# Optimization experiments

Hardware: AMD Instinct MI355X
Metric: run time of the kernel (lower is better)

The kernel has to match this reference:

```python
import jax, jax.numpy as jnp
import numpy as np


def setup_inputs() -> dict:
    key = jax.random.key(0)
    k1, k2, k3, k4 = jax.random.split(key, 4)
    tokens, d_in, d_out = 8192, 4096, 4096
    x = jax.random.normal(k1, (tokens, d_in), dtype=jnp.float32)
    # int8-valued weights stored as int32 for portability; values in [-128, 127]
    quantized_weights = jax.random.randint(k2, (d_out, d_in), -128, 128, dtype=jnp.int32)
    scales = jax.random.uniform(k3, (d_out,), dtype=jnp.float32) * 0.02 + 1e-4
    bias = jax.random.normal(k4, (d_out,), dtype=jnp.float32)
    return {"x": x, "quantized_weights": quantized_weights, "scales": scales, "bias": bias}


def reference(x, quantized_weights, scales, bias):
    # dequantize-on-the-fly linear: (x @ W_q^T) * scales + bias
    w = quantized_weights.astype(x.dtype)                # [out, in]
    out = jnp.einsum('ti,oi->to', x, w)                  # [tokens, out]
    out = out * scales[None, :].astype(x.dtype)
    out = out + bias.astype(x.dtype)
    return out
```

## Files before the change

### kernel.cpp

```cpp
#include <hip/hip_runtime.h>
#include <stdint.h>

#define M_TOK 8192
#define N_OUT 4096
#define K_IN  4096

#define BM 256
#define BN 256
#define BK 128
#define NT (K_IN / BK)
#define SEC 16384
#define BUF 65536

typedef int intx4 __attribute__((ext_vector_type(4)));

#define MFMAI8 __builtin_amdgcn_mfma_i32_16x16x64_i8


__device__ __forceinline__ void async_copy16(const void* g, void* l) {
    __builtin_amdgcn_global_load_lds(
        (__attribute__((address_space(1))) void*)(g),
        (__attribute__((address_space(3))) void*)(l),
        16, 0, 0);
}


#define NWB 4096

__global__ void prep_kernel(const float* __restrict__ x,
                            const int* __restrict__ wq,
                            int8_t* __restrict__ xq,
                            float* __restrict__ sx,
                            int8_t* __restrict__ wb) {
    const int tid = threadIdx.x;

    if (blockIdx.x < M_TOK) {
        const int row = blockIdx.x;
        const float4* p = (const float4*)(x + (size_t)row * K_IN + tid * 16);
        float4 v0 = p[0], v1 = p[1], v2 = p[2], v3 = p[3];

        float m = fabsf(v0.x);
        m = fmaxf(m, fabsf(v0.y)); m = fmaxf(m, fabsf(v0.z)); m = fmaxf(m, fabsf(v0.w));
        m = fmaxf(m, fabsf(v1.x)); m = fmaxf(m, fabsf(v1.y));
        m = fmaxf(m, fabsf(v1.z)); m = fmaxf(m, fabsf(v1.w));
        m = fmaxf(m, fabsf(v2.x)); m = fmaxf(m, fabsf(v2.y));
        m = fmaxf(m, fabsf(v2.z)); m = fmaxf(m, fabsf(v2.w));
        m = fmaxf(m, fabsf(v3.x)); m = fmaxf(m, fabsf(v3.y));
        m = fmaxf(m, fabsf(v3.z)); m = fmaxf(m, fabsf(v3.w));

#pragma unroll
        for (int off = 32; off; off >>= 1) m = fmaxf(m, __shfl_xor(m, off));
        __shared__ float wmax[4];
        if ((tid & 63) == 0) wmax[tid >> 6] = m;
        __syncthreads();
        m = fmaxf(fmaxf(wmax[0], wmax[1]), fmaxf(wmax[2], wmax[3]));
        m = fmaxf(m, 1e-20f);

        const float rs = 127.0f / m;
        if (tid == 0) sx[row] = m * (1.0f / 127.0f);

        union { int4 v; int8_t c[16]; } u;
        u.c[0]  = (int8_t)__float2int_rn(v0.x * rs);
        u.c[1]  = (int8_t)__float2int_rn(v0.y * rs);
        u.c[2]  = (int8_t)__float2int_rn(v0.z * rs);
        u.c[3]  = (int8_t)__float2int_rn(v0.w * rs);
        u.c[4]  = (int8_t)__float2int_rn(v1.x * rs);
        u.c[5]  = (int8_t)__float2int_rn(v1.y * rs);
        u.c[6]  = (int8_t)__float2int_rn(v1.z * rs);
        u.c[7]  = (int8_t)__float2int_rn(v1.w * rs);
        u.c[8]  = (int8_t)__float2int_rn(v2.x * rs);
        u.c[9]  = (int8_t)__float2int_rn(v2.y * rs);
        u.c[10] = (int8_t)__float2int_rn(v2.z * rs);
        u.c[11] = (int8_t)__float2int_rn(v2.w * rs);
        u.c[12] = (int8_t)__float2int_rn(v3.x * rs);
        u.c[13] = (int8_t)__float2int_rn(v3.y * rs);
        u.c[14] = (int8_t)__float2int_rn(v3.z * rs);
        u.c[15] = (int8_t)__float2int_rn(v3.w * rs);
        ((int4*)(xq + (size_t)row * K_IN))[tid] = u.v;
    } else {
        const int i = (blockIdx.x - M_TOK) * 256 + tid;
        const int4* p = (const int4*)wq + (size_t)i * 4;
        int4 a = p[0], b = p[1], c = p[2], d = p[3];
        union { int4 v; int8_t q[16]; } u;
        u.q[0]  = (int8_t)a.x; u.q[1]  = (int8_t)a.y; u.q[2]  = (int8_t)a.z; u.q[3]  = (int8_t)a.w;
        u.q[4]  = (int8_t)b.x; u.q[5]  = (int8_t)b.y; u.q[6]  = (int8_t)b.z; u.q[7]  = (int8_t)b.w;
        u.q[8]  = (int8_t)c.x; u.q[9]  = (int8_t)c.y; u.q[10] = (int8_t)c.z; u.q[11] = (int8_t)c.w;
        u.q[12] = (int8_t)d.x; u.q[13] = (int8_t)d.y; u.q[14] = (int8_t)d.z; u.q[15] = (int8_t)d.w;
        ((int4*)wb)[i] = u.v;
    }
}


__global__ __launch_bounds__(512, 2)
void gemm_i8_kernel(const int8_t* __restrict__ A,
                    const int8_t* __restrict__ B,
                    const float* __restrict__ sx,
                    const float* __restrict__ scales,
                    const float* __restrict__ bias,
                    float* __restrict__ C) {
    __shared__ __align__(16) int8_t lds[2 * BUF];

    const int tid = threadIdx.x;

    const int nwg = (M_TOK / BM) * (N_OUT / BN);
    const int cpx = nwg / 8;
    const int wg  = (blockIdx.x % 8) * cpx + blockIdx.x / 8;
    const int bn  = wg & 15;
    const int bm  = wg >> 4;

    const int lane = tid & 63;
    const int wave = tid >> 6;
    const int wm   = wave >> 2;
    const int wn   = wave & 3;

    const int t8 = tid >> 3;
    const int cg = (tid & 7) ^ (t8 & 7);
    const int grow0 = 2 * t8 + (cg >> 2);
    const int gcol0 = (cg & 3) * 16;
    const int8_t* aP = A + (size_t)(bm * BM + grow0) * K_IN + gcol0;
    const int8_t* bP = B + (size_t)(bn * BN + grow0) * K_IN + gcol0;

    auto stA = [&](int tt, int s) {
        int8_t* d = &lds[(tt & 1) * BUF + s * SEC + tid * 16];
        const int8_t* g = aP + (size_t)tt * BK + s * 64;
        async_copy16(g, d);
        async_copy16(g + (size_t)128 * K_IN, d + 8192);
    };
    auto stB = [&](int tt, int s) {
        int8_t* d = &lds[(tt & 1) * BUF + 2 * SEC + s * SEC + tid * 16];
        const int8_t* g = bP + (size_t)tt * BK + s * 64;
        async_copy16(g, d);
        async_copy16(g + (size_t)128 * K_IN, d + 8192);
    };

    const int r16 = lane & 15;
    const int q   = lane >> 4;
    const int cr  = (((r16 & 1) << 2) + q) ^ ((r16 >> 1) & 7);
    const int aOff = (wm * 64 + (r16 >> 1)) * 128 + cr * 16;
    const int bOff = 2 * SEC + (wn * 32 + (r16 >> 1)) * 128 + cr * 16;

    intx4 acc[8][4] = {};
    intx4 afA[4], afB[4], bfA[4], bfB[4];

#define RD_A03(dst, base, s)                                                   \
    { _Pragma("unroll") for (int i = 0; i < 4; ++i)                            \
        dst[i] = *(const intx4*)((base) + (s) * SEC + aOff + i * 1024); }
#define RD_A47(dst, base, s)                                                   \
    { _Pragma("unroll") for (int i = 0; i < 4; ++i)                            \
        dst[i] = *(const intx4*)((base) + (s) * SEC + aOff + (4 + i) * 1024); }
#define RD_BF(dst, base, s)                                                    \
    { _Pragma("unroll") for (int j = 0; j < 4; ++j)                            \
        dst[j] = *(const intx4*)((base) + (s) * SEC + bOff + j * 1024); }
#define MM03(af, bf)                                                           \
    { __builtin_amdgcn_s_setprio(1);                                           \
      _Pragma("unroll") for (int i = 0; i < 4; ++i)                            \
          _Pragma("unroll") for (int j = 0; j < 4; ++j)                        \
              acc[i][j] = MFMAI8(af[i], bf[j], acc[i][j], 0, 0, 0);            \
      __builtin_amdgcn_s_setprio(0); }
#define MM47(af, bf)                                                           \
    { __builtin_amdgcn_s_setprio(1);                                           \
      _Pragma("unroll") for (int i = 0; i < 4; ++i)                            \
          _Pragma("unroll") for (int j = 0; j < 4; ++j)                        \
              acc[4 + i][j] = MFMAI8(af[i], bf[j], acc[4 + i][j], 0, 0, 0);    \
      __builtin_amdgcn_s_setprio(0); }
#define SBAR __builtin_amdgcn_sched_barrier(0)

    stA(0, 0); stB(0, 0); stA(0, 1); stB(0, 1);
    asm volatile("s_waitcnt vmcnt(0)" ::: "memory");
    __builtin_amdgcn_s_barrier();
    asm volatile("" ::: "memory");
    RD_A03(afA, lds, 0);
    RD_BF(bfA, lds, 0);

#pragma unroll 1
    for (int t = 0; t < NT; ++t) {
        const int8_t* Lb  = lds + (t & 1) * BUF;
        const int8_t* Lb2 = lds + ((t + 1) & 1) * BUF;
        const bool pf = (t + 1 < NT);

        if (pf) { stA(t + 1, 0); stA(t + 1, 1); }
        RD_A47(afB, Lb, 0);
        asm volatile("s_waitcnt lgkmcnt(4)" ::: "memory");
        SBAR;
        MM03(afA, bfA);

        if (pf) { stB(t + 1, 0); stB(t + 1, 1); }
        RD_A03(afA, Lb, 1);
        RD_BF(bfB, Lb, 1);
        asm volatile("s_waitcnt lgkmcnt(8)" ::: "memory");
        SBAR;
        MM47(afB, bfA);

        RD_A47(afB, Lb, 1);
        asm volatile("s_waitcnt lgkmcnt(4)" ::: "memory");
        SBAR;
        MM03(afA, bfB);

        asm volatile("s_waitcnt vmcnt(0) lgkmcnt(0)" ::: "memory");
        __builtin_amdgcn_s_barrier();
        asm volatile("" ::: "memory");
        if (pf) {
            RD_A03(afA, Lb2, 0);
            RD_BF(bfA, Lb2, 0);
        }
        SBAR;
        MM47(afB, bfB);
    }

    const int row0 = bm * BM + wm * 128 + q * 4;
    const int col0 = bn * BN + wn * 64 + r16;
    float sxv[8][4];
#pragma unroll
    for (int fr = 0; fr < 8; ++fr)
#pragma unroll
        for (int r = 0; r < 4; ++r)
            sxv[fr][r] = sx[row0 + fr * 16 + r];
#pragma unroll
    for (int fc = 0; fc < 4; ++fc) {
        const int n  = col0 + fc * 16;
        const float sc = scales[n];
        const float bi = bias[n];
#pragma unroll
        for (int fr = 0; fr < 8; ++fr) {
            const int m = row0 + fr * 16;
#pragma unroll
            for (int r = 0; r < 4; ++r)
                C[(size_t)(m + r) * N_OUT + n] =
                    (float)acc[fr][fc][r] * (sxv[fr][r] * sc) + bi;
        }
    }
}


extern "C" void kernel_launch(void* const* d_in, const int* in_sizes, int n_in,
                              void* d_out, int out_size, void* d_ws, size_t ws_size,
                              hipStream_t stream) {
    const float* x      = (const float*)d_in[0];
    const int*   wq     = (const int*)d_in[1];
    const float* scales = (const float*)d_in[2];
    const float* bias   = (const float*)d_in[3];
    float*       out    = (float*)d_out;

    int8_t* xq = (int8_t*)d_ws;
    int8_t* wb = xq + (size_t)M_TOK * K_IN;
    float*  sx = (float*)(wb + (size_t)N_OUT * K_IN);

    prep_kernel<<<M_TOK + NWB, 256, 0, stream>>>(x, wq, xq, sx, wb);

    const int grid = (M_TOK / BM) * (N_OUT / BN);
    gemm_i8_kernel<<<grid, 512, 0, stream>>>(xq, wb, sx, scales, bias, out);
}
```

Measured before the change: 188.6 us.

## Switch int8 GEMM to 32x32x32 MFMA with new LDS slice layout

Replaces the 16x16x64 int8 MFMA tiles with 32x32x32 int8 MFMA instructions, using 4x2 accumulators of 16 ints per wave in place of 8x4 of 4. The LDS staging is reorganised into four 32-byte K-slices per operand, with a new XOR swizzle and per-lane read offsets matched to the larger fragment shape. The epilogue now reads sx per element instead of preloading it. The intent is to cut instruction issue overhead and raise MFMA throughput per LDS read, at the risk of new bank conflicts and scattered epilogue loads.

New measurement: 224.8 us. 19.2% more time.

```diff
diff --git a/kernel.cpp b/kernel.cpp
--- a/kernel.cpp
+++ b/kernel.cpp
@@ -9,12 +9,14 @@
 #define BN 256
 #define BK 128
 #define NT (K_IN / BK)
-#define SEC 16384
-#define BUF 65536
-
-typedef int intx4 __attribute__((ext_vector_type(4)));
-
-#define MFMAI8 __builtin_amdgcn_mfma_i32_16x16x64_i8
+#define SLICE 8192
+#define BSEC  32768
+#define BUF   65536
+
+typedef int intx4  __attribute__((ext_vector_type(4)));
+typedef int intx16 __attribute__((ext_vector_type(16)));
+
+#define MFMA32 __builtin_amdgcn_mfma_i32_32x32x32_i8
 
 
 __device__ __forceinline__ void async_copy16(const void* g, void* l) {
@@ -113,64 +115,53 @@
     const int wm   = wave >> 2;
     const int wn   = wave & 3;
 
-    const int t8 = tid >> 3;
-    const int cg = (tid & 7) ^ (t8 & 7);
-    const int grow0 = 2 * t8 + (cg >> 2);
-    const int gcol0 = (cg & 3) * 16;
-    const int8_t* aP = A + (size_t)(bm * BM + grow0) * K_IN + gcol0;
-    const int8_t* bP = B + (size_t)(bn * BN + grow0) * K_IN + gcol0;
+    const int grow0 = ((tid >> 6) << 5) + ((tid >> 1) & 31);
+    const int gc0   = (((tid & 1) ^ ((tid >> 3) & 1)) << 4);
+    const int8_t* aP = A + (size_t)(bm * BM + grow0) * K_IN + gc0;
+    const int8_t* bP = B + (size_t)(bn * BN + grow0) * K_IN + gc0;
 
     auto stA = [&](int tt, int s) {
-        int8_t* d = &lds[(tt & 1) * BUF + s * SEC + tid * 16];
-        const int8_t* g = aP + (size_t)tt * BK + s * 64;
-        async_copy16(g, d);
-        async_copy16(g + (size_t)128 * K_IN, d + 8192);
+        async_copy16(aP + (size_t)tt * BK + s * 32,
+                     &lds[(tt & 1) * BUF + s * SLICE + tid * 16]);
     };
     auto stB = [&](int tt, int s) {
-        int8_t* d = &lds[(tt & 1) * BUF + 2 * SEC + s * SEC + tid * 16];
-        const int8_t* g = bP + (size_t)tt * BK + s * 64;
-        async_copy16(g, d);
-        async_copy16(g + (size_t)128 * K_IN, d + 8192);
+        async_copy16(bP + (size_t)tt * BK + s * 32,
+                     &lds[(tt & 1) * BUF + BSEC + s * SLICE + tid * 16]);
     };
 
-    const int r16 = lane & 15;
-    const int q   = lane >> 4;
-    const int cr  = (((r16 & 1) << 2) + q) ^ ((r16 >> 1) & 7);
-    const int aOff = (wm * 64 + (r16 >> 1)) * 128 + cr * 16;
-    const int bOff = 2 * SEC + (wn * 32 + (r16 >> 1)) * 128 + cr * 16;
-
-    intx4 acc[8][4] = {};
+    const int aRd = ((lane & 31) << 5) + ((((lane >> 5) ^ (lane >> 2)) & 1) << 4);
+    const int hi  = lane >> 5;
+
+    intx16 acc[4][2] = {};
     intx4 afA[4], afB[4], bfA[4], bfB[4];
 
-#define RD_A03(dst, base, s)                                                   \
-    { _Pragma("unroll") for (int i = 0; i < 4; ++i)                            \
-        dst[i] = *(const intx4*)((base) + (s) * SEC + aOff + i * 1024); }
-#define RD_A47(dst, base, s)                                                   \
-    { _Pragma("unroll") for (int i = 0; i < 4; ++i)                            \
-        dst[i] = *(const intx4*)((base) + (s) * SEC + aOff + (4 + i) * 1024); }
-#define RD_BF(dst, base, s)                                                    \
-    { _Pragma("unroll") for (int j = 0; j < 4; ++j)                            \
-        dst[j] = *(const intx4*)((base) + (s) * SEC + bOff + j * 1024); }
-#define MM03(af, bf)                                                           \
+#define RD_A(dst, base, sp, f0)                                                \
+    { _Pragma("unroll") for (int fr = 0; fr < 2; ++fr)                         \
+        _Pragma("unroll") for (int ss = 0; ss < 2; ++ss)                       \
+            dst[fr * 2 + ss] = *(const intx4*)((base) +                        \
+                ((sp) * 2 + ss) * SLICE + (wm * 4 + (f0) + fr) * 1024 + aRd); }
+#define RD_B(dst, base, sp)                                                    \
+    { _Pragma("unroll") for (int fc = 0; fc < 2; ++fc)                         \
+        _Pragma("unroll") for (int ss = 0; ss < 2; ++ss)                       \
+            dst[fc * 2 + ss] = *(const intx4*)((base) + BSEC +                 \
+                ((sp) * 2 + ss) * SLICE + (wn * 2 + fc) * 1024 + aRd); }
+#define MM(af, bf, a0)                                                         \
     { __builtin_amdgcn_s_setprio(1);                                           \
-      _Pragma("unroll") for (int i = 0; i < 4; ++i)                            \
-          _Pragma("unroll") for (int j = 0; j < 4; ++j)                        \
-              acc[i][j] = MFMAI8(af[i], bf[j], acc[i][j], 0, 0, 0);            \
-      __builtin_amdgcn_s_setprio(0); }
-#define MM47(af, bf)                                                           \
-    { __builtin_amdgcn_s_setprio(1);                                           \
-      _Pragma("unroll") for (int i = 0; i < 4; ++i)                            \
-          _Pragma("unroll") for (int j = 0; j < 4; ++j)                        \
-              acc[4 + i][j] = MFMAI8(af[i], bf[j], acc[4 + i][j], 0, 0, 0);    \
+      _Pragma("unroll") for (int fr = 0; fr < 2; ++fr)                         \
+          _Pragma("unroll") for (int fc = 0; fc < 2; ++fc)                     \
+              _Pragma("unroll") for (int ss = 0; ss < 2; ++ss)                 \
+                  acc[(a0) + fr][fc] = MFMA32(af[fr * 2 + ss],                 \
+                      bf[fc * 2 + ss], acc[(a0) + fr][fc], 0, 0, 0);           \
       __builtin_amdgcn_s_setprio(0); }
 #define SBAR __builtin_amdgcn_sched_barrier(0)
 
-    stA(0, 0); stB(0, 0); stA(0, 1); stB(0, 1);
+    stA(0, 0); stA(0, 1); stA(0, 2); stA(0, 3);
+    stB(0, 0); stB(0, 1); stB(0, 2); stB(0, 3);
     asm volatile("s_waitcnt vmcnt(0)" ::: "memory");
     __builtin_amdgcn_s_barrier();
     asm volatile("" ::: "memory");
-    RD_A03(afA, lds, 0);
-    RD_BF(bfA, lds, 0);
+    RD_A(afA, lds, 0, 0);
+    RD_B(bfA, lds, 0);
 
 #pragma unroll 1
     for (int t = 0; t < NT; ++t) {
@@ -178,55 +169,51 @@
         const int8_t* Lb2 = lds + ((t + 1) & 1) * BUF;
         const bool pf = (t + 1 < NT);
 
-        if (pf) { stA(t + 1, 0); stA(t + 1, 1); }
-        RD_A47(afB, Lb, 0);
+        if (pf) { stA(t + 1, 0); stA(t + 1, 1); stA(t + 1, 2); stA(t + 1, 3); }
+        RD_A(afB, Lb, 0, 2);
         asm volatile("s_waitcnt lgkmcnt(4)" ::: "memory");
         SBAR;
-        MM03(afA, bfA);
-
-        if (pf) { stB(t + 1, 0); stB(t + 1, 1); }
-        RD_A03(afA, Lb, 1);
-        RD_BF(bfB, Lb, 1);
+        MM(afA, bfA, 0);
+
+        if (pf) { stB(t + 1, 0); stB(t + 1, 1); stB(t + 1, 2); stB(t + 1, 3); }
+        RD_A(afA, Lb, 1, 0);
+        RD_B(bfB, Lb, 1);
         asm volatile("s_waitcnt lgkmcnt(8)" ::: "memory");
         SBAR;
-        MM47(afB, bfA);
-
-        RD_A47(afB, Lb, 1);
+        MM(afB, bfA, 2);
+
+        RD_A(afB, Lb, 1, 2);
         asm volatile("s_waitcnt lgkmcnt(4)" ::: "memory");
         SBAR;
-        MM03(afA, bfB);
+        MM(afA, bfB, 0);
 
         asm volatile("s_waitcnt vmcnt(0) lgkmcnt(0)" ::: "memory");
         __builtin_amdgcn_s_barrier();
         asm volatile("" ::: "memory");
         if (pf) {
-            RD_A03(afA, Lb2, 0);
-            RD_BF(bfA, Lb2, 0);
+            RD_A(afA, Lb2, 0, 0);
+            RD_B(bfA, Lb2, 0);
         }
         SBAR;
-        MM47(afB, bfB);
+        MM(afB, bfB, 2);
     }
 
-    const int row0 = bm * BM + wm * 128 + q * 4;
-    const int col0 = bn * BN + wn * 64 + r16;
-    float sxv[8][4];
-#pragma unroll
-    for (int fr = 0; fr < 8; ++fr)
-#pragma unroll
-        for (int r = 0; r < 4; ++r)
-            sxv[fr][r] = sx[row0 + fr * 16 + r];
-#pragma unroll
-    for (int fc = 0; fc < 4; ++fc) {
-        const int n  = col0 + fc * 16;
+    const int row0 = bm * BM + wm * 128 + 4 * hi;
+    const int col0 = bn * BN + wn * 64 + (lane & 31);
+#pragma unroll
+    for (int fc = 0; fc < 2; ++fc) {
+        const int n  = col0 + fc * 32;
         const float sc = scales[n];
         const float bi = bias[n];
 #pragma unroll
-        for (int fr = 0; fr < 8; ++fr) {
-            const int m = row0 + fr * 16;
-#pragma unroll
-            for (int r = 0; r < 4; ++r)
-                C[(size_t)(m + r) * N_OUT + n] =
-                    (float)acc[fr][fc][r] * (sxv[fr][r] * sc) + bi;
+        for (int fr = 0; fr < 4; ++fr) {
+            const int mb = row0 + fr * 32;
+#pragma unroll
+            for (int reg = 0; reg < 16; ++reg) {
+                const int m = mb + (reg & 3) + 8 * (reg >> 2);
+                C[(size_t)m * N_OUT + n] =
+                    (float)acc[fr][fc][reg] * (sx[m] * sc) + bi;
+            }
         }
     }
 }
```
